# Kernel tuning notes

Measured on AMD Instinct MI355X. Metric: run time of the kernel, lower is better.

The kernel has to match this reference:

```python
import jax, jax.numpy as jnp
import numpy as np

N_NODES = 20000
N_EDGES = 320000
F_IN = 128
H = 4        # heads per layer
D = 128      # per-head hidden dim
NEG_SLOPE = 0.2


def setup_inputs() -> dict:
    key = jax.random.key(0)
    ks = jax.random.split(key, 14)
    s = 0.05
    inp = {
        "feats": jax.random.normal(ks[0], (N_NODES, F_IN), jnp.float32),
        "src": jax.random.randint(ks[1], (N_EDGES,), 0, N_NODES, jnp.int64),
        "dst": jax.random.randint(ks[2], (N_EDGES,), 0, N_NODES, jnp.int64),
        # layer 1: in F_IN -> H heads x D, flatten agg
        "W1": s * jax.random.normal(ks[3], (F_IN, H * D), jnp.float32),
        "al1": s * jax.random.normal(ks[4], (H, D), jnp.float32),
        "ar1": s * jax.random.normal(ks[5], (H, D), jnp.float32),
        "b1": jnp.zeros((H * D,), jnp.float32),
        # layer 2: in H*D -> H heads x D, mean agg
        "W2": s * jax.random.normal(ks[6], (H * D, H * D), jnp.float32),
        "al2": s * jax.random.normal(ks[7], (H, D), jnp.float32),
        "ar2": s * jax.random.normal(ks[8], (H, D), jnp.float32),
        "b2": jnp.zeros((H * D,), jnp.float32),
        # readout Linear(D, 1)
        "Wr": s * jax.random.normal(ks[9], (D, 1), jnp.float32),
        "br": jnp.zeros((1,), jnp.float32),
    }
    return inp


def _gat_conv(x, src, dst, W, al, ar, b, n_nodes):
    """dgl GATConv: per-head linear, edge softmax over incoming edges, scatter-sum."""
    h, d = al.shape
    z = (x @ W).reshape(n_nodes, h, d)                      # [N,H,D]
    el = jnp.einsum('nhd,hd->nh', z, al)                    # [N,H]
    er = jnp.einsum('nhd,hd->nh', z, ar)                    # [N,H]
    e = jax.nn.leaky_relu(el[src] + er[dst], NEG_SLOPE)     # [E,H]
    # numerically stable softmax grouped by destination node
    emax = jax.lax.stop_gradient(jax.ops.segment_max(e, dst, num_segments=n_nodes))
    a = jnp.exp(e - emax[dst])                              # [E,H]
    denom = jax.ops.segment_sum(a, dst, num_segments=n_nodes)
    alpha = a / jnp.maximum(denom[dst], 1e-9)               # [E,H]
    out = jax.ops.segment_sum(alpha[:, :, None] * z[src], dst, num_segments=n_nodes)
    return out + b.reshape(1, h, d)                         # [N,H,D]


def reference(feats, src, dst, W1, al1, ar1, b1, W2, al2, ar2, b2, Wr, br):
    n = feats.shape[0]
    h1 = _gat_conv(feats, src, dst, W1, al1, ar1, b1, n)    # [N,H,D]
    h1 = jax.nn.elu(h1.reshape(n, -1))                      # flatten heads -> [N,H*D]
    h2 = _gat_conv(h1, src, dst, W2, al2, ar2, b2, n)       # [N,H,D]
    h2 = h2.mean(axis=1)                                    # mean over heads -> [N,D]
    node_preds = h2 @ Wr + br                               # [N,1]
    return node_preds.sum(axis=0)                           # [1]
```

## Files before the change

### kernel.cpp

```cpp
#include <hip/hip_runtime.h>
#include <hip/hip_bf16.h>
#include <cstddef>

constexpr int NN = 20000;
constexpr int NE = 320000;
constexpr int NHEAD = 4;
constexpr int ND = 128;
constexpr int HD = 512;
constexpr int MPAD = 20096;
constexpr int SLOTS = 64;
constexpr float NEG_SLOPE = 0.2f;

using short8 = __attribute__((ext_vector_type(8))) short;
using f32x4 = __attribute__((ext_vector_type(4))) float;
using f32x2 = __attribute__((ext_vector_type(2))) float;

__device__ inline void gload16(const void* g, void* l) {
  __builtin_amdgcn_global_load_lds(
      (const __attribute__((address_space(1))) void*)g,
      (__attribute__((address_space(3))) void*)l, 16, 0, 0);
}

__device__ inline unsigned char f32_to_fp8(float v) {
  int pk = __builtin_amdgcn_cvt_pk_fp8_f32(v, v, 0, false);
  return (unsigned char)(pk & 0xff);
}

constexpr int S0 = NN;
constexpr int S1 = S0 + MPAD * 128;
constexpr int S2 = S1 + 512 * 128;
constexpr int S3 = S2 + 12 * 512;
constexpr int S4 = S3 + 256;
__global__ __launch_bounds__(256) void prep_kernel(
    const float* __restrict__ feats, const float* __restrict__ W1,
    const float* __restrict__ W2, const float* __restrict__ al2,
    const float* __restrict__ ar2, const float* __restrict__ Wr,
    __hip_bfloat16* __restrict__ featsb, __hip_bfloat16* __restrict__ W1t,
    float* __restrict__ vcomb, float* __restrict__ partials,
    int* __restrict__ cnt) {
  int t = blockIdx.x * 256 + threadIdx.x;
  if (t < S0) {
    cnt[t] = 0;
  } else if (t < S1) {
    int u = t - S0;
    featsb[u] = __float2bfloat16(u < NN * 128 ? feats[u] : 0.f);
  } else if (t < S2) {
    int u = t - S1;
    W1t[u] = __float2bfloat16(W1[(size_t)(u & 127) * 512 + (u >> 7)]);
  } else if (t < S3) {
    int u = t - S2;
    int v = u >> 9, k = u & 511;
    int h = (v < 4) ? v : (v < 8) ? v - 4 : v - 8;
    const float* vec = (v < 4) ? (al2 + h * 128)
                     : (v < 8) ? (ar2 + h * 128) : Wr;
    const float* wrow = W2 + (size_t)k * 512 + h * 128;
    float s = 0.f;
    for (int d = 0; d < 128; ++d) s += wrow[d] * vec[d];
    vcomb[u] = s;
  } else if (t < S4) {
    partials[t - S3] = 0.f;
  }
}

__global__ __launch_bounds__(256) void gemm1_kernel(
    const __hip_bfloat16* __restrict__ A,
    const __hip_bfloat16* __restrict__ Bt,
    unsigned char* __restrict__ C,
    const float* __restrict__ al, const float* __restrict__ ar,
    float* __restrict__ el, float* __restrict__ er,
    const int* __restrict__ src, const int* __restrict__ dst,
    int* __restrict__ cnt, int* __restrict__ src_perm) {
  constexpr int K = 128;
  __shared__ short As[128 * 32];
  __shared__ short Bs[128 * 32];
  __shared__ float elbuf[4][128];
  __shared__ float erbuf[4][128];
  int t = threadIdx.x;

  {
    int nth = gridDim.x * gridDim.y * 256;
    int gid = (blockIdx.y * gridDim.x + blockIdx.x) * 256 + t;
    for (int e = gid; e < NE; e += nth) {
      int d = dst[e];
      int p = atomicAdd(&cnt[d], 1);
      if (p < SLOTS) src_perm[d * SLOTS + p] = src[e];
    }
  }

  int lane = t & 63;
  int wave = t >> 6;
  int rowBase = blockIdx.x * 128;
  int head = blockIdx.y;
  int colBase = head * 128;
  int woffr = (wave & 1) * 64;
  int woffc = (wave >> 1) * 64;
  int mrow = lane & 15, quad = lane >> 4;

  f32x4 acc[4][4];
#pragma unroll
  for (int i = 0; i < 4; ++i)
#pragma unroll
    for (int j = 0; j < 4; ++j) acc[i][j] = (f32x4){0.f, 0.f, 0.f, 0.f};

  for (int k0 = 0; k0 < K; k0 += 32) {
#pragma unroll
    for (int p = 0; p < 2; ++p) {
      int f = p * 256 + wave * 64 + lane;
      int r = f >> 2, kc = f & 3;
      gload16(A + (size_t)(rowBase + r) * K + k0 + kc * 8,
              As + p * 2048 + wave * 512);
      gload16(Bt + (size_t)(colBase + r) * K + k0 + kc * 8,
              Bs + p * 2048 + wave * 512);
    }
    __syncthreads();
    short8 af[4], bfr[4];
#pragma unroll
    for (int i = 0; i < 4; ++i)
      af[i] = *(const short8*)&As[(woffr + i * 16 + mrow) * 32 + quad * 8];
#pragma unroll
    for (int j = 0; j < 4; ++j)
      bfr[j] = *(const short8*)&Bs[(woffc + j * 16 + mrow) * 32 + quad * 8];
#pragma unroll
    for (int i = 0; i < 4; ++i)
#pragma unroll
      for (int j = 0; j < 4; ++j)
        acc[i][j] = __builtin_amdgcn_mfma_f32_16x16x32_bf16(af[i], bfr[j], acc[i][j], 0, 0, 0);
    __syncthreads();
  }

#pragma unroll
  for (int i = 0; i < 4; ++i) {
#pragma unroll
    for (int j = 0; j < 4; ++j) {
      int col = colBase + woffc + j * 16 + mrow;
#pragma unroll
      for (int r = 0; r < 4; ++r) {
        int row = rowBase + woffr + i * 16 + quad * 4 + r;
        C[(size_t)row * HD + col] = f32_to_fp8(acc[i][j][r]);
      }
    }
  }

  float al_v[4], ar_v[4];
#pragma unroll
  for (int j = 0; j < 4; ++j) {
    int coll = woffc + j * 16 + mrow;
    al_v[j] = al[head * 128 + coll];
    ar_v[j] = ar[head * 128 + coll];
  }
#pragma unroll
  for (int i = 0; i < 4; ++i) {
#pragma unroll
    for (int r = 0; r < 4; ++r) {
      float pl = 0.f, pr = 0.f;
#pragma unroll
      for (int j = 0; j < 4; ++j) {
        float v = acc[i][j][r];
        pl += v * al_v[j];
        pr += v * ar_v[j];
      }
#pragma unroll
      for (int off = 1; off < 16; off <<= 1) {
        pl += __shfl_xor(pl, off);
        pr += __shfl_xor(pr, off);
      }
      if (mrow == 0) {
        int row128 = woffr + i * 16 + quad * 4 + r;
        elbuf[wave][row128] = pl;
        erbuf[wave][row128] = pr;
      }
    }
  }
  __syncthreads();
  if (t < 128) {
    int row = t;
    int w0 = (row < 64) ? 0 : 1;
    float ev = elbuf[w0][row] + elbuf[w0 + 2][row];
    float rv = erbuf[w0][row] + erbuf[w0 + 2][row];
    int gr = rowBase + row;
    if (gr < NN) {
      el[gr * 4 + head] = ev;
      er[gr * 4 + head] = rv;
    }
  }
}

__global__ __launch_bounds__(256) void aggregate_kernel(
    const unsigned char* __restrict__ zf8,
    const int* __restrict__ cnt,
    const int* __restrict__ src_perm,
    const float* __restrict__ el,
    const float* __restrict__ er,
    const float* __restrict__ b1,
    const float* __restrict__ vcomb,
    float* __restrict__ el2,
    float* __restrict__ er2,
    float* __restrict__ q2) {
  __shared__ float aldsT[4][4][66];
  int wv = __builtin_amdgcn_readfirstlane((int)(threadIdx.x >> 6));
  int n = blockIdx.x * 4 + wv;
  int lane = threadIdx.x & 63;
  int c = min(cnt[n], SLOTS);
  int base = n * SLOTS;

  {
    float4 er4 = *reinterpret_cast<const float4*>(&er[n * 4]);
    float a0 = 0.f, a1 = 0.f, a2 = 0.f, a3 = 0.f;
    if (lane < c) {
      int s = src_perm[base + lane];
      float4 e4 = *reinterpret_cast<const float4*>(&el[s * 4]);
      float x0 = e4.x + er4.x, x1 = e4.y + er4.y;
      float x2 = e4.z + er4.z, x3 = e4.w + er4.w;
      x0 = (x0 > 0.f) ? x0 : NEG_SLOPE * x0;
      x1 = (x1 > 0.f) ? x1 : NEG_SLOPE * x1;
      x2 = (x2 > 0.f) ? x2 : NEG_SLOPE * x2;
      x3 = (x3 > 0.f) ? x3 : NEG_SLOPE * x3;
      a0 = __expf(x0); a1 = __expf(x1); a2 = __expf(x2); a3 = __expf(x3);
    }
    float s0 = a0, s1 = a1, s2 = a2, s3 = a3;
#pragma unroll
    for (int off = 1; off < 64; off <<= 1) {
      s0 += __shfl_xor(s0, off);
      s1 += __shfl_xor(s1, off);
      s2 += __shfl_xor(s2, off);
      s3 += __shfl_xor(s3, off);
    }
    aldsT[wv][0][lane] = a0 / fmaxf(s0, 1e-9f);
    aldsT[wv][1][lane] = a1 / fmaxf(s1, 1e-9f);
    aldsT[wv][2][lane] = a2 / fmaxf(s2, 1e-9f);
    aldsT[wv][3][lane] = a3 / fmaxf(s3, 1e-9f);
  }

  int head = lane >> 4;
  const float* arow = &aldsT[wv][head][0];
  float acc[8] = {};

#define EDGE_BODY(IDX)                                                         \
  {                                                                            \
    int s = src_perm[base + (IDX)];                                            \
    float a = arow[(IDX)];                                                     \
    uint2 w = *reinterpret_cast<const uint2*>(zf8 + (size_t)s * 512 + lane * 8); \
    f32x2 f0 = __builtin_amdgcn_cvt_pk_f32_fp8(w.x, false);                    \
    f32x2 f1 = __builtin_amdgcn_cvt_pk_f32_fp8(w.x, true);                     \
    f32x2 f2 = __builtin_amdgcn_cvt_pk_f32_fp8(w.y, false);                    \
    f32x2 f3 = __builtin_amdgcn_cvt_pk_f32_fp8(w.y, true);                     \
    acc[0] += a * f0.x; acc[1] += a * f0.y;                                    \
    acc[2] += a * f1.x; acc[3] += a * f1.y;                                    \
    acc[4] += a * f2.x; acc[5] += a * f2.y;                                    \
    acc[6] += a * f3.x; acc[7] += a * f3.y;                                    \
  }

  int i = 0;
  for (; i + 7 < c; i += 8) {
    EDGE_BODY(i)
    EDGE_BODY(i + 1)
    EDGE_BODY(i + 2)
    EDGE_BODY(i + 3)
    EDGE_BODY(i + 4)
    EDGE_BODY(i + 5)
    EDGE_BODY(i + 6)
    EDGE_BODY(i + 7)
  }
  for (; i < c; ++i) EDGE_BODY(i)
#undef EDGE_BODY

  float4 bA = *reinterpret_cast<const float4*>(&b1[lane * 8]);
  float4 bB = *reinterpret_cast<const float4*>(&b1[lane * 8 + 4]);
  float v[8];
  v[0] = acc[0] + bA.x; v[1] = acc[1] + bA.y;
  v[2] = acc[2] + bA.z; v[3] = acc[3] + bA.w;
  v[4] = acc[4] + bB.x; v[5] = acc[5] + bB.y;
  v[6] = acc[6] + bB.z; v[7] = acc[7] + bB.w;
#pragma unroll
  for (int j = 0; j < 8; ++j) v[j] = (v[j] > 0.f) ? v[j] : expm1f(v[j]);

  float r[12];
#pragma unroll
  for (int vv = 0; vv < 12; ++vv) {
    const float* vb = vcomb + vv * 512 + lane * 8;
    float4 cA = *reinterpret_cast<const float4*>(vb);
    float4 cB = *reinterpret_cast<const float4*>(vb + 4);
    float p = v[0] * cA.x + v[1] * cA.y + v[2] * cA.z + v[3] * cA.w +
              v[4] * cB.x + v[5] * cB.y + v[6] * cB.z + v[7] * cB.w;
#pragma unroll
    for (int off = 1; off < 64; off <<= 1) p += __shfl_xor(p, off);
    r[vv] = p;
  }
  if (lane == 0) {
    *reinterpret_cast<float4*>(&el2[n * 4]) = make_float4(r[0], r[1], r[2], r[3]);
    *reinterpret_cast<float4*>(&er2[n * 4]) = make_float4(r[4], r[5], r[6], r[7]);
    *reinterpret_cast<float4*>(&q2[n * 4]) = make_float4(r[8], r[9], r[10], r[11]);
  }
}

__global__ __launch_bounds__(256) void attn_q_kernel(
    const int* __restrict__ src_perm,
    const int* __restrict__ cnt,
    const float* __restrict__ el,
    const float* __restrict__ er,
    const float* __restrict__ q,
    float* __restrict__ partials) {
  __shared__ float blk[4];
  int wv = __builtin_amdgcn_readfirstlane((int)(threadIdx.x >> 6));
  int n = blockIdx.x * 4 + wv;
  int lane = threadIdx.x & 63;
  int c = min(cnt[n], SLOTS);
  float4 er4 = *reinterpret_cast<const float4*>(&er[n * 4]);
  float a0 = 0.f, a1 = 0.f, a2 = 0.f, a3 = 0.f;
  int s = 0;
  if (lane < c) {
    s = src_perm[n * SLOTS + lane];
    float4 e4 = *reinterpret_cast<const float4*>(&el[s * 4]);
    float x0 = e4.x + er4.x, x1 = e4.y + er4.y;
    float x2 = e4.z + er4.z, x3 = e4.w + er4.w;
    x0 = (x0 > 0.f) ? x0 : NEG_SLOPE * x0;
    x1 = (x1 > 0.f) ? x1 : NEG_SLOPE * x1;
    x2 = (x2 > 0.f) ? x2 : NEG_SLOPE * x2;
    x3 = (x3 > 0.f) ? x3 : NEG_SLOPE * x3;
    a0 = __expf(x0); a1 = __expf(x1); a2 = __expf(x2); a3 = __expf(x3);
  }
  float s0 = a0, s1 = a1, s2 = a2, s3 = a3;
#pragma unroll
  for (int off = 1; off < 64; off <<= 1) {
    s0 += __shfl_xor(s0, off);
    s1 += __shfl_xor(s1, off);
    s2 += __shfl_xor(s2, off);
    s3 += __shfl_xor(s3, off);
  }
  float p = 0.f;
  if (lane < c) {
    float4 q4 = *reinterpret_cast<const float4*>(&q[s * 4]);
    p = (a0 / fmaxf(s0, 1e-9f)) * q4.x + (a1 / fmaxf(s1, 1e-9f)) * q4.y +
        (a2 / fmaxf(s2, 1e-9f)) * q4.z + (a3 / fmaxf(s3, 1e-9f)) * q4.w;
  }
#pragma unroll
  for (int off = 32; off > 0; off >>= 1) p += __shfl_down(p, off);
  if (lane == 0) blk[wv] = p;
  __syncthreads();
  if (threadIdx.x == 0) {
    atomicAdd(&partials[blockIdx.x & 255], blk[0] + blk[1] + blk[2] + blk[3]);
  }
}

__global__ __launch_bounds__(512) void final_kernel(
    const float* __restrict__ partials, const float* __restrict__ b2,
    const float* __restrict__ Wr, const float* __restrict__ br,
    float* __restrict__ out) {
  __shared__ float tmp[512];
  int t = threadIdx.x;
  float sum = (t < 256) ? partials[t] : 0.f;
  sum += (float)NN * b2[t] * Wr[t & 127];
  tmp[t] = sum;
  __syncthreads();
  for (int off = 256; off > 0; off >>= 1) {
    if (t < off) tmp[t] += tmp[t + off];
    __syncthreads();
  }
  if (t == 0) out[0] = 0.25f * tmp[0] + (float)NN * br[0];
}

extern "C" void kernel_launch(void* const* d_in, const int* in_sizes, int n_in,
                              void* d_out, int out_size, void* d_ws, size_t ws_size,
                              hipStream_t stream) {
  const float* feats = (const float*)d_in[0];
  const int* src = (const int*)d_in[1];
  const int* dst = (const int*)d_in[2];
  const float* W1 = (const float*)d_in[3];
  const float* al1 = (const float*)d_in[4];
  const float* ar1 = (const float*)d_in[5];
  const float* b1 = (const float*)d_in[6];
  const float* W2 = (const float*)d_in[7];
  const float* al2 = (const float*)d_in[8];
  const float* ar2 = (const float*)d_in[9];
  const float* b2 = (const float*)d_in[10];
  const float* Wr = (const float*)d_in[11];
  const float* br = (const float*)d_in[12];
  float* out = (float*)d_out;

  __hip_bfloat16* featsb = (__hip_bfloat16*)d_ws;
  unsigned char* zf8 = (unsigned char*)(featsb + (size_t)MPAD * 128);
  __hip_bfloat16* W1t = (__hip_bfloat16*)(zf8 + (size_t)MPAD * HD);
  float* vcomb = (float*)(W1t + 512 * 128);
  float* el1 = vcomb + 12 * 512;
  float* er1 = el1 + (size_t)NN * NHEAD;
  float* el2 = er1 + (size_t)NN * NHEAD;
  float* er2 = el2 + (size_t)NN * NHEAD;
  float* q2 = er2 + (size_t)NN * NHEAD;
  float* partials = q2 + (size_t)NN * NHEAD;
  int* cnt = (int*)(partials + 256 + 4);
  int* src_perm = cnt + NN;

  prep_kernel<<<(S4 + 255) / 256, 256, 0, stream>>>(
      feats, W1, W2, al2, ar2, Wr, featsb, W1t, vcomb, partials, cnt);

  dim3 gemm_grid(MPAD / 128, NHEAD);

  gemm1_kernel<<<gemm_grid, 256, 0, stream>>>(featsb, W1t, zf8, al1, ar1,
                                              el1, er1, src, dst, cnt, src_perm);

  aggregate_kernel<<<NN / 4, 256, 0, stream>>>(zf8, cnt, src_perm, el1, er1, b1,
                                               vcomb, el2, er2, q2);

  attn_q_kernel<<<NN / 4, 256, 0, stream>>>(src_perm, cnt, el2, er2, q2, partials);
  final_kernel<<<1, 512, 0, stream>>>(partials, b2, Wr, br, out);
}
```

Measured before the change: 176.4 us.

## Split layer-1 features per head and remap aggregation blocks to XCDs by head

The fp8 layer-1 features are now stored head-major, one [MPAD,128] slab per head. Aggregation launches one block per (head, 4-node group) and maps blocks so each pair of XCDs handles a single head, which shrinks each XCD's gather working set so it fits better in L2. Each wave gathers four edges at once with 16 lanes per edge and then combines the partial sums with shuffles. The projection to layer-2 el/er/q is moved into a separate kernel that reads a bf16 copy of h1, which adds a kernel launch and an extra round trip of h1 through memory.

After: 246.0 us. 1.39x slower.

```diff
diff --git a/kernel.cpp b/kernel.cpp
--- a/kernel.cpp
+++ b/kernel.cpp
@@ -65,7 +65,7 @@
 __global__ __launch_bounds__(256) void gemm1_kernel(
     const __hip_bfloat16* __restrict__ A,
     const __hip_bfloat16* __restrict__ Bt,
-    unsigned char* __restrict__ C,
+    unsigned char* __restrict__ zh,
     const float* __restrict__ al, const float* __restrict__ ar,
     float* __restrict__ el, float* __restrict__ er,
     const int* __restrict__ src, const int* __restrict__ dst,
@@ -128,15 +128,16 @@
     __syncthreads();
   }
 
+  unsigned char* zreg = zh + (size_t)head * MPAD * 128;
 #pragma unroll
   for (int i = 0; i < 4; ++i) {
 #pragma unroll
     for (int j = 0; j < 4; ++j) {
-      int col = colBase + woffc + j * 16 + mrow;
+      int colh = woffc + j * 16 + mrow;
 #pragma unroll
       for (int r = 0; r < 4; ++r) {
         int row = rowBase + woffr + i * 16 + quad * 4 + r;
-        C[(size_t)row * HD + col] = f32_to_fp8(acc[i][j][r]);
+        zreg[(size_t)row * 128 + colh] = f32_to_fp8(acc[i][j][r]);
       }
     }
   }
@@ -186,102 +187,108 @@
 }
 
 __global__ __launch_bounds__(256) void aggregate_kernel(
-    const unsigned char* __restrict__ zf8,
+    const unsigned char* __restrict__ zh,
     const int* __restrict__ cnt,
     const int* __restrict__ src_perm,
     const float* __restrict__ el,
     const float* __restrict__ er,
     const float* __restrict__ b1,
-    const float* __restrict__ vcomb,
-    float* __restrict__ el2,
-    float* __restrict__ er2,
-    float* __restrict__ q2) {
-  __shared__ float aldsT[4][4][66];
+    __hip_bfloat16* __restrict__ h1b) {
+  __shared__ float alds[4][SLOTS];
+  int bid = blockIdx.x;
+  int xcd = bid & 7;
+  int head = xcd >> 1;
+  int grp = (bid >> 3) * 2 + (xcd & 1);
   int wv = __builtin_amdgcn_readfirstlane((int)(threadIdx.x >> 6));
-  int n = blockIdx.x * 4 + wv;
+  int n = grp * 4 + wv;
   int lane = threadIdx.x & 63;
   int c = min(cnt[n], SLOTS);
   int base = n * SLOTS;
 
   {
-    float4 er4 = *reinterpret_cast<const float4*>(&er[n * 4]);
-    float a0 = 0.f, a1 = 0.f, a2 = 0.f, a3 = 0.f;
+    float ern = er[n * 4 + head];
+    float a = 0.f;
     if (lane < c) {
       int s = src_perm[base + lane];
-      float4 e4 = *reinterpret_cast<const float4*>(&el[s * 4]);
-      float x0 = e4.x + er4.x, x1 = e4.y + er4.y;
-      float x2 = e4.z + er4.z, x3 = e4.w + er4.w;
-      x0 = (x0 > 0.f) ? x0 : NEG_SLOPE * x0;
-      x1 = (x1 > 0.f) ? x1 : NEG_SLOPE * x1;
-      x2 = (x2 > 0.f) ? x2 : NEG_SLOPE * x2;
-      x3 = (x3 > 0.f) ? x3 : NEG_SLOPE * x3;
-      a0 = __expf(x0); a1 = __expf(x1); a2 = __expf(x2); a3 = __expf(x3);
-    }
-    float s0 = a0, s1 = a1, s2 = a2, s3 = a3;
-#pragma unroll
-    for (int off = 1; off < 64; off <<= 1) {
-      s0 += __shfl_xor(s0, off);
-      s1 += __shfl_xor(s1, off);
-      s2 += __shfl_xor(s2, off);
-      s3 += __shfl_xor(s3, off);
-    }
-    aldsT[wv][0][lane] = a0 / fmaxf(s0, 1e-9f);
-    aldsT[wv][1][lane] = a1 / fmaxf(s1, 1e-9f);
-    aldsT[wv][2][lane] = a2 / fmaxf(s2, 1e-9f);
-    aldsT[wv][3][lane] = a3 / fmaxf(s3, 1e-9f);
-  }
-
-  int head = lane >> 4;
-  const float* arow = &aldsT[wv][head][0];
+      float x = el[s * 4 + head] + ern;
+      x = (x > 0.f) ? x : NEG_SLOPE * x;
+      a = __expf(x);
+    }
+    float ssum = a;
+#pragma unroll
+    for (int off = 1; off < 64; off <<= 1) ssum += __shfl_xor(ssum, off);
+    alds[wv][lane] = a / fmaxf(ssum, 1e-9f);
+  }
+
+  int g = lane >> 4, li = lane & 15;
+  const unsigned char* zbase = zh + (size_t)head * MPAD * 128 + li * 8;
   float acc[8] = {};
 
-#define EDGE_BODY(IDX)                                                         \
-  {                                                                            \
-    int s = src_perm[base + (IDX)];                                            \
-    float a = arow[(IDX)];                                                     \
-    uint2 w = *reinterpret_cast<const uint2*>(zf8 + (size_t)s * 512 + lane * 8); \
+#define EDGE_BODY(E)                                                           \
+  if ((E) < c) {                                                               \
+    int s = src_perm[base + (E)];                                              \
+    float aa = alds[wv][(E)];                                                  \
+    uint2 w = *reinterpret_cast<const uint2*>(zbase + (size_t)s * 128);        \
     f32x2 f0 = __builtin_amdgcn_cvt_pk_f32_fp8(w.x, false);                    \
     f32x2 f1 = __builtin_amdgcn_cvt_pk_f32_fp8(w.x, true);                     \
     f32x2 f2 = __builtin_amdgcn_cvt_pk_f32_fp8(w.y, false);                    \
     f32x2 f3 = __builtin_amdgcn_cvt_pk_f32_fp8(w.y, true);                     \
-    acc[0] += a * f0.x; acc[1] += a * f0.y;                                    \
-    acc[2] += a * f1.x; acc[3] += a * f1.y;                                    \
-    acc[4] += a * f2.x; acc[5] += a * f2.y;                                    \
-    acc[6] += a * f3.x; acc[7] += a * f3.y;                                    \
-  }
-
-  int i = 0;
-  for (; i + 7 < c; i += 8) {
-    EDGE_BODY(i)
-    EDGE_BODY(i + 1)
-    EDGE_BODY(i + 2)
-    EDGE_BODY(i + 3)
-    EDGE_BODY(i + 4)
-    EDGE_BODY(i + 5)
-    EDGE_BODY(i + 6)
-    EDGE_BODY(i + 7)
-  }
-  for (; i < c; ++i) EDGE_BODY(i)
+    acc[0] += aa * f0.x; acc[1] += aa * f0.y;                                  \
+    acc[2] += aa * f1.x; acc[3] += aa * f1.y;                                  \
+    acc[4] += aa * f2.x; acc[5] += aa * f2.y;                                  \
+    acc[6] += aa * f3.x; acc[7] += aa * f3.y;                                  \
+  }
+
+  for (int i = 0; i < c; i += 8) {
+    EDGE_BODY(i + g)
+    EDGE_BODY(i + 4 + g)
+  }
 #undef EDGE_BODY
 
-  float4 bA = *reinterpret_cast<const float4*>(&b1[lane * 8]);
-  float4 bB = *reinterpret_cast<const float4*>(&b1[lane * 8 + 4]);
+#pragma unroll
+  for (int j = 0; j < 8; ++j) {
+    acc[j] += __shfl_xor(acc[j], 16);
+    acc[j] += __shfl_xor(acc[j], 32);
+  }
+
   float v[8];
-  v[0] = acc[0] + bA.x; v[1] = acc[1] + bA.y;
-  v[2] = acc[2] + bA.z; v[3] = acc[3] + bA.w;
-  v[4] = acc[4] + bB.x; v[5] = acc[5] + bB.y;
-  v[6] = acc[6] + bB.z; v[7] = acc[7] + bB.w;
-#pragma unroll
-  for (int j = 0; j < 8; ++j) v[j] = (v[j] > 0.f) ? v[j] : expm1f(v[j]);
-
+#pragma unroll
+  for (int j = 0; j < 8; ++j) {
+    float x = acc[j] + b1[head * 128 + li * 8 + j];
+    v[j] = (x > 0.f) ? x : expm1f(x);
+  }
+  if (lane < 16) {
+    __hip_bfloat162 o[4];
+#pragma unroll
+    for (int j = 0; j < 4; ++j)
+      o[j] = __float22bfloat162_rn(make_float2(v[2 * j], v[2 * j + 1]));
+    *reinterpret_cast<uint4*>(h1b + (size_t)n * HD + head * 128 + li * 8) =
+        *reinterpret_cast<const uint4*>(o);
+  }
+}
+
+__global__ __launch_bounds__(256) void proj_kernel(
+    const __hip_bfloat16* __restrict__ h1b,
+    const float* __restrict__ vcomb,
+    float* __restrict__ el2, float* __restrict__ er2,
+    float* __restrict__ q2) {
+  int wv = __builtin_amdgcn_readfirstlane((int)(threadIdx.x >> 6));
+  int n = blockIdx.x * 4 + wv;
+  int lane = threadIdx.x & 63;
+  const __hip_bfloat162* hp =
+      reinterpret_cast<const __hip_bfloat162*>(h1b + (size_t)n * HD + lane * 8);
+  float2 h0 = __bfloat1622float2(hp[0]);
+  float2 h1 = __bfloat1622float2(hp[1]);
+  float2 h2 = __bfloat1622float2(hp[2]);
+  float2 h3 = __bfloat1622float2(hp[3]);
   float r[12];
 #pragma unroll
   for (int vv = 0; vv < 12; ++vv) {
     const float* vb = vcomb + vv * 512 + lane * 8;
     float4 cA = *reinterpret_cast<const float4*>(vb);
     float4 cB = *reinterpret_cast<const float4*>(vb + 4);
-    float p = v[0] * cA.x + v[1] * cA.y + v[2] * cA.z + v[3] * cA.w +
-              v[4] * cB.x + v[5] * cB.y + v[6] * cB.z + v[7] * cB.w;
+    float p = h0.x * cA.x + h0.y * cA.y + h1.x * cA.z + h1.y * cA.w +
+              h2.x * cB.x + h2.y * cB.y + h3.x * cB.z + h3.y * cB.w;
 #pragma unroll
     for (int off = 1; off < 64; off <<= 1) p += __shfl_xor(p, off);
     r[vv] = p;
@@ -378,8 +385,9 @@
   float* out = (float*)d_out;
 
   __hip_bfloat16* featsb = (__hip_bfloat16*)d_ws;
-  unsigned char* zf8 = (unsigned char*)(featsb + (size_t)MPAD * 128);
-  __hip_bfloat16* W1t = (__hip_bfloat16*)(zf8 + (size_t)MPAD * HD);
+  unsigned char* zh = (unsigned char*)(featsb + (size_t)MPAD * 128);
+  __hip_bfloat16* h1b = (__hip_bfloat16*)(zh + (size_t)MPAD * HD);
+  __hip_bfloat16* W1t = h1b + (size_t)MPAD * HD;
   float* vcomb = (float*)(W1t + 512 * 128);
   float* el1 = vcomb + 12 * 512;
   float* er1 = el1 + (size_t)NN * NHEAD;
@@ -395,11 +403,12 @@
 
   dim3 gemm_grid(MPAD / 128, NHEAD);
 
-  gemm1_kernel<<<gemm_grid, 256, 0, stream>>>(featsb, W1t, zf8, al1, ar1,
+  gemm1_kernel<<<gemm_grid, 256, 0, stream>>>(featsb, W1t, zh, al1, ar1,
                                               el1, er1, src, dst, cnt, src_perm);
 
-  aggregate_kernel<<<NN / 4, 256, 0, stream>>>(zf8, cnt, src_perm, el1, er1, b1,
-                                               vcomb, el2, er2, q2);
+  aggregate_kernel<<<NN, 256, 0, stream>>>(zh, cnt, src_perm, el1, er1, b1, h1b);
+
+  proj_kernel<<<NN / 4, 256, 0, stream>>>(h1b, vcomb, el2, er2, q2);
 
   attn_q_kernel<<<NN / 4, 256, 0, stream>>>(src_perm, cnt, el2, er2, q2, partials);
   final_kernel<<<1, 512, 0, stream>>>(partials, b2, Wr, br, out);
```
